# Optimization experiments

Hardware: AMD Instinct MI355X
Metric: run time of the kernel (lower is better)

Reference implementation:

```python
import jax, jax.numpy as jnp
import numpy as np

N = 100000   # nodes
E = 600000   # edges
B = 512      # graphs in batch
H = 128      # hidden dim
ED = 8       # edge feature dim
TWO48 = float(2 ** 48 - 1)


def _w(k, shape, fan_in):
    return jax.random.normal(k, shape, jnp.float32) * (1.0 / np.sqrt(fan_in))


def setup_inputs() -> dict:
    key = jax.random.key(0)
    ks = jax.random.split(key, 32)
    inp = {}
    inp["s_node_ids"] = jax.random.randint(ks[0], (N,), 0, 2 ** 31 - 1, dtype=jnp.int32)
    inp["s_edge_index"] = jax.random.randint(ks[1], (2, E), 0, N, dtype=jnp.int32)
    inp["s_edge_attr"] = jax.random.normal(ks[2], (E, ED), jnp.float32)
    inp["s_batch"] = jnp.sort(jax.random.randint(ks[3], (N,), 0, B, dtype=jnp.int32))
    inp["depth"] = jax.random.uniform(ks[4], (B,), jnp.float32)
    # id_mlp: Linear(1,H) -> ReLU -> Linear(H,H)
    inp["id_w1"] = _w(ks[5], (1, H), 1); inp["id_b1"] = jnp.zeros((H,), jnp.float32)
    inp["id_w2"] = _w(ks[6], (H, H), H); inp["id_b2"] = jnp.zeros((H,), jnp.float32)
    # edge_mlp: Linear(ED,H) -> ReLU -> Linear(H,H)
    inp["ed_w1"] = _w(ks[7], (ED, H), ED); inp["ed_b1"] = jnp.zeros((H,), jnp.float32)
    inp["ed_w2"] = _w(ks[8], (H, H), H); inp["ed_b2"] = jnp.zeros((H,), jnp.float32)
    # GINEConv nn MLPs: Linear(H,H) -> ReLU -> Linear(H,H)
    inp["c1_w1"] = _w(ks[9], (H, H), H); inp["c1_b1"] = jnp.zeros((H,), jnp.float32)
    inp["c1_w2"] = _w(ks[10], (H, H), H); inp["c1_b2"] = jnp.zeros((H,), jnp.float32)
    inp["c2_w1"] = _w(ks[11], (H, H), H); inp["c2_b1"] = jnp.zeros((H,), jnp.float32)
    inp["c2_w2"] = _w(ks[12], (H, H), H); inp["c2_b2"] = jnp.zeros((H,), jnp.float32)
    inp["rg_w1"] = _w(ks[13], (H + 1, H), H + 1); inp["rg_b1"] = jnp.zeros((H,), jnp.float32)
    inp["rg_w2"] = _w(ks[14], (H, 1), H); inp["rg_b2"] = jnp.zeros((1,), jnp.float32)
    return inp


def _mlp2(x, w1, b1, w2, b2):
    return jax.nn.relu(x @ w1 + b1) @ w2 + b2


def _gine(x, src, dst, e, w1, b1, w2, b2):
    # message = ReLU(x_j + e), sum-aggregated at dst; out = nn((1+eps)*x + aggr), eps=0
    msg = jax.nn.relu(x[src] + e)                       # [E, H]
    aggr = jax.ops.segment_sum(msg, dst, num_segments=N)  # [N, H]
    return _mlp2(x + aggr, w1, b1, w2, b2)


def _global_mean(x, batch):
    sums = jax.ops.segment_sum(x, batch, num_segments=B)                          # [B, H]
    cnts = jax.ops.segment_sum(jnp.ones((x.shape[0], 1), x.dtype), batch, num_segments=B)
    return sums / jnp.maximum(cnts, 1.0)


def reference(s_node_ids, s_edge_index, s_edge_attr, s_batch, depth,
              id_w1, id_b1, id_w2, id_b2,
              ed_w1, ed_b1, ed_w2, ed_b2,
              c1_w1, c1_b1, c1_w2, c1_b2,
              c2_w1, c2_b1, c2_w2, c2_b2,
              rg_w1, rg_b1, rg_w2, rg_b2):
    src, dst = s_edge_index[0], s_edge_index[1]
    x0 = jnp.clip(s_node_ids.astype(jnp.float32) / TWO48, 0.0, 1.0)[:, None]  # [N,1]
    x = _mlp2(x0, id_w1, id_b1, id_w2, id_b2)                                 # [N,H]
    e = _mlp2(s_edge_attr, ed_w1, ed_b1, ed_w2, ed_b2)                        # [E,H]
    x = jax.nn.relu(_gine(x, src, dst, e, c1_w1, c1_b1, c1_w2, c1_b2))
    x = jax.nn.relu(_gine(x, src, dst, e, c2_w1, c2_b1, c2_w2, c2_b2))
    rep = jnp.concatenate([_global_mean(x, s_batch), depth[:, None]], axis=1)  # [B,H+1]
    return _mlp2(rep, rg_w1, rg_b1, rg_w2, rg_b2)[:, 0]                        # [B]
```

## Files before the change

kernel.cpp:

```cpp
#include <hip/hip_runtime.h>
#include <hip/hip_bf16.h>

#define N_NODES 100000
#define N_EDGES 600000
#define NB      512
#define H       128
#define ED      8
#define SCAN_CHUNK 1024
#define N_CHUNKS   98

typedef __attribute__((ext_vector_type(8))) short short8;
typedef __attribute__((ext_vector_type(4))) float f32x4;
typedef unsigned short u16;
typedef unsigned int   u32;

static __device__ __forceinline__ u16 f2bf(float f) {
    u32 u = __float_as_uint(f);
    u32 r = u + 0x7fffu + ((u >> 16) & 1u);
    return (u16)(r >> 16);
}
static __device__ __forceinline__ float bf2f(u32 h) {
    return __uint_as_float(h << 16);
}

__global__ __launch_bounds__(256) void pack_all_kernel(
    const float* __restrict__ W0, const float* __restrict__ W1,
    const float* __restrict__ W2, const float* __restrict__ W3,
    const float* __restrict__ W4, const float* __restrict__ W5,
    const float* __restrict__ W6,
    short8* __restrict__ O0, short8* __restrict__ O1,
    short8* __restrict__ O2, short8* __restrict__ O3,
    short8* __restrict__ O4, short8* __restrict__ O5,
    short8* __restrict__ O6)
{
    int gid = blockIdx.x * 256 + threadIdx.x;
    const int total = 512 + 6 * 2048;
    if (gid >= total) return;
    const float* W; short8* O; int Krows, kkmax, slot;
    if (gid < 512) { W = W0; O = O0; Krows = ED; kkmax = 1; slot = gid; }
    else {
        int m = (gid - 512) / 2048;
        slot = (gid - 512) % 2048;
        Krows = H; kkmax = 4;
        switch (m) {
            case 0: W = W1; O = O1; break;
            case 1: W = W2; O = O2; break;
            case 2: W = W3; O = O3; break;
            case 3: W = W4; O = O4; break;
            case 4: W = W5; O = O5; break;
            default: W = W6; O = O6; break;
        }
    }
    int lane = slot & 63;
    int t = slot >> 6;
    int nt = t & 1; t >>= 1;
    int kk = t % kkmax;
    int w  = t / kkmax;
    int quad = lane >> 4, n15 = lane & 15;
    int n = w * 32 + nt * 16 + n15;
    short8 v;
    #pragma unroll
    for (int j = 0; j < 8; j++) {
        int k = kk * 32 + quad * 8 + j;
        v[j] = (k < Krows) ? (short)f2bf(W[k * H + n]) : (short)0;
    }
    O[slot] = v;
}

__global__ __launch_bounds__(256) void hist_kernel(
    const int* __restrict__ edge_index, int* __restrict__ counts)
{
    int e = blockIdx.x * 256 + threadIdx.x;
    if (e < N_EDGES) atomicAdd(&counts[edge_index[N_EDGES + e]], 1);
}

__global__ __launch_bounds__(SCAN_CHUNK) void scan1_kernel(
    const int* __restrict__ counts, int* __restrict__ chunk_scan,
    int* __restrict__ bsum_raw)
{
    __shared__ int s[SCAN_CHUNK];
    int tid = threadIdx.x;
    int gid = blockIdx.x * SCAN_CHUNK + tid;
    int v = counts[gid];
    s[tid] = v;
    __syncthreads();
    #pragma unroll
    for (int off = 1; off < SCAN_CHUNK; off <<= 1) {
        int t = (tid >= off) ? s[tid - off] : 0;
        __syncthreads();
        s[tid] += t;
        __syncthreads();
    }
    chunk_scan[gid] = s[tid] - v;
    if (tid == SCAN_CHUNK - 1) bsum_raw[blockIdx.x] = s[tid];
}

__global__ __launch_bounds__(128) void scan2_kernel(
    const int* __restrict__ bsum_raw, int* __restrict__ bsum_scan)
{
    __shared__ int s[128];
    int tid = threadIdx.x;
    int v = (tid < N_CHUNKS) ? bsum_raw[tid] : 0;
    s[tid] = v;
    __syncthreads();
    #pragma unroll
    for (int off = 1; off < 128; off <<= 1) {
        int t = (tid >= off) ? s[tid - off] : 0;
        __syncthreads();
        s[tid] += t;
        __syncthreads();
    }
    bsum_scan[tid] = s[tid] - v;
}

__global__ __launch_bounds__(256) void fill_kernel(
    const int* __restrict__ edge_index,
    const int* __restrict__ chunk_scan, const int* __restrict__ bsum_scan,
    int* __restrict__ counts, int* __restrict__ src_list,
    int* __restrict__ pos_of)
{
    int e = blockIdx.x * 256 + threadIdx.x;
    if (e >= N_EDGES) return;
    int src = edge_index[e];
    int dst = edge_index[N_EDGES + e];
    int slot = atomicAdd(&counts[dst], -1) - 1;
    int pos = chunk_scan[dst] + bsum_scan[dst >> 10] + slot;
    src_list[pos] = src;
    pos_of[e] = pos;
}

__global__ __launch_bounds__(256) void node_mlp_mfma(
    const int* __restrict__ ids,
    const float* __restrict__ w1, const float* __restrict__ b1,
    const short8* __restrict__ pW2, const float* __restrict__ b2,
    u16* __restrict__ x_out)
{
    __shared__ u16 sH[64 * 136];
    __shared__ float s_x0[64];
    int tid = threadIdx.x;
    int w = tid >> 6, lane = tid & 63, quad = lane >> 4, n15 = lane & 15;
    short8 fW2[4][2];
    #pragma unroll
    for (int kk = 0; kk < 4; kk++) {
        fW2[kk][0] = pW2[((w * 4 + kk) * 2 + 0) * 64 + lane];
        fW2[kk][1] = pW2[((w * 4 + kk) * 2 + 1) * 64 + lane];
    }
    float rb2[2] = { b2[w * 32 + n15], b2[w * 32 + 16 + n15] };
    float w1c = w1[tid & 127], b1c = b1[tid & 127];
    const int ntile = (N_NODES + 63) / 64;
    for (int tile = blockIdx.x; tile < ntile; tile += gridDim.x) {
        int row0 = tile * 64;
        if (tid < 64) {
            int n = row0 + tid;
            float x0 = (n < N_NODES) ? (float)ids[n] / 281474976710655.0f : 0.0f;
            s_x0[tid] = fminf(fmaxf(x0, 0.0f), 1.0f);
        }
        __syncthreads();
        int half = tid >> 7, c = tid & 127;
        #pragma unroll 8
        for (int rr = 0; rr < 32; rr++) {
            int r = half + rr * 2;
            sH[r * 136 + c] = f2bf(fmaxf(s_x0[r] * w1c + b1c, 0.0f));
        }
        __syncthreads();
        f32x4 acc[4][2];
        #pragma unroll
        for (int s = 0; s < 4; s++) { acc[s][0] = (f32x4){0,0,0,0}; acc[s][1] = (f32x4){0,0,0,0}; }
        #pragma unroll
        for (int kk = 0; kk < 4; kk++) {
            #pragma unroll
            for (int s = 0; s < 4; s++) {
                short8 a = *(const short8*)&sH[(s * 16 + n15) * 136 + kk * 32 + quad * 8];
                acc[s][0] = __builtin_amdgcn_mfma_f32_16x16x32_bf16(a, fW2[kk][0], acc[s][0], 0, 0, 0);
                acc[s][1] = __builtin_amdgcn_mfma_f32_16x16x32_bf16(a, fW2[kk][1], acc[s][1], 0, 0, 0);
            }
        }
        #pragma unroll
        for (int s = 0; s < 4; s++)
            #pragma unroll
            for (int nt = 0; nt < 2; nt++) {
                int col = w * 32 + nt * 16 + n15;
                #pragma unroll
                for (int reg = 0; reg < 4; reg++) {
                    int n = row0 + s * 16 + quad * 4 + reg;
                    if (n < N_NODES)
                        x_out[(long)n * H + col] = f2bf(acc[s][nt][reg] + rb2[nt]);
                }
            }
        __syncthreads();
    }
}

__global__ __launch_bounds__(256) void edge_mlp_mfma(
    const float* __restrict__ attr,
    const int* __restrict__ pos_of,
    const short8* __restrict__ pW1, const float* __restrict__ b1,
    const short8* __restrict__ pW2, const float* __restrict__ b2,
    u16* __restrict__ e_perm)
{
    __shared__ u16 sA[64 * 40];
    __shared__ u16 sH[64 * 136];
    __shared__ int sPos[64];
    int tid = threadIdx.x;
    int w = tid >> 6, lane = tid & 63, quad = lane >> 4, n15 = lane & 15;
    short8 fW1[2];
    fW1[0] = pW1[(w * 2 + 0) * 64 + lane];
    fW1[1] = pW1[(w * 2 + 1) * 64 + lane];
    short8 fW2[4][2];
    #pragma unroll
    for (int kk = 0; kk < 4; kk++) {
        fW2[kk][0] = pW2[((w * 4 + kk) * 2 + 0) * 64 + lane];
        fW2[kk][1] = pW2[((w * 4 + kk) * 2 + 1) * 64 + lane];
    }
    float rb1[2] = { b1[w * 32 + n15], b1[w * 32 + 16 + n15] };
    float rb2[2] = { b2[w * 32 + n15], b2[w * 32 + 16 + n15] };
    const int ntile = N_EDGES / 64;
    for (int tile = blockIdx.x; tile < ntile; tile += gridDim.x) {
        int row0 = tile * 64;
        if (tid < 64) sPos[tid] = pos_of[row0 + tid];
        if (tid >= 64 && tid < 192) {
            int t2 = tid - 64;
            int r = t2 >> 1, c4 = (t2 & 1) * 4;
            float4 v = *(const float4*)&attr[(long)(row0 + r) * ED + c4];
            ushort4 o;
            o.x = f2bf(v.x); o.y = f2bf(v.y); o.z = f2bf(v.z); o.w = f2bf(v.w);
            *(ushort4*)&sA[r * 40 + c4] = o;
        } else if (tid >= 192) {
            int idx = tid - 192;
            for (; idx < 192; idx += 64) {
                int r = idx / 3, c8 = 8 + (idx % 3) * 8;
                *(uint4*)&sA[r * 40 + c8] = make_uint4(0, 0, 0, 0);
            }
        }
        __syncthreads();
        f32x4 acc[4][2];
        #pragma unroll
        for (int s = 0; s < 4; s++) { acc[s][0] = (f32x4){0,0,0,0}; acc[s][1] = (f32x4){0,0,0,0}; }
        #pragma unroll
        for (int s = 0; s < 4; s++) {
            short8 a = *(const short8*)&sA[(s * 16 + n15) * 40 + quad * 8];
            acc[s][0] = __builtin_amdgcn_mfma_f32_16x16x32_bf16(a, fW1[0], acc[s][0], 0, 0, 0);
            acc[s][1] = __builtin_amdgcn_mfma_f32_16x16x32_bf16(a, fW1[1], acc[s][1], 0, 0, 0);
        }
        #pragma unroll
        for (int s = 0; s < 4; s++)
            #pragma unroll
            for (int nt = 0; nt < 2; nt++) {
                int col = w * 32 + nt * 16 + n15;
                #pragma unroll
                for (int reg = 0; reg < 4; reg++)
                    sH[(s * 16 + quad * 4 + reg) * 136 + col] =
                        f2bf(fmaxf(acc[s][nt][reg] + rb1[nt], 0.0f));
            }
        __syncthreads();
        #pragma unroll
        for (int s = 0; s < 4; s++) { acc[s][0] = (f32x4){0,0,0,0}; acc[s][1] = (f32x4){0,0,0,0}; }
        #pragma unroll
        for (int kk = 0; kk < 4; kk++) {
            #pragma unroll
            for (int s = 0; s < 4; s++) {
                short8 a = *(const short8*)&sH[(s * 16 + n15) * 136 + kk * 32 + quad * 8];
                acc[s][0] = __builtin_amdgcn_mfma_f32_16x16x32_bf16(a, fW2[kk][0], acc[s][0], 0, 0, 0);
                acc[s][1] = __builtin_amdgcn_mfma_f32_16x16x32_bf16(a, fW2[kk][1], acc[s][1], 0, 0, 0);
            }
        }
        #pragma unroll
        for (int s = 0; s < 4; s++)
            #pragma unroll
            for (int nt = 0; nt < 2; nt++) {
                int col = w * 32 + nt * 16 + n15;
                #pragma unroll
                for (int reg = 0; reg < 4; reg++) {
                    long r = sPos[s * 16 + quad * 4 + reg];
                    e_perm[r * H + col] = f2bf(acc[s][nt][reg] + rb2[nt]);
                }
            }
        __syncthreads();
    }
}

__global__ __launch_bounds__(256) void aggregate_kernel(
    const int* __restrict__ src_list,
    const int* __restrict__ chunk_scan, const int* __restrict__ bsum_scan,
    const u16* __restrict__ e_perm,
    const u16* __restrict__ x,
    u16* __restrict__ xs_out)
{
    int wave = threadIdx.x >> 6;
    int lane = threadIdx.x & 63;
    int fo = lane * 2;
    const int ngroups = N_NODES / 4;
    for (int g = blockIdx.x; g < ngroups; g += gridDim.x) {
        int n = g * 4 + wave;
        int beg = chunk_scan[n]     + bsum_scan[n >> 10];
        int end = chunk_scan[n + 1] + bsum_scan[(n + 1) >> 10];
        float a0 = 0.0f, a1 = 0.0f;
        for (int j0 = beg; j0 < end; j0 += 64) {
            int m = min(64, end - j0);
            int sv = (lane < m) ? src_list[j0 + lane] : 0;
            for (int j = 0; j < m; j++) {
                int src = __shfl(sv, j);
                u32 xv = *(const u32*)&x[(long)src * H + fo];
                u32 ev = *(const u32*)&e_perm[(long)(j0 + j) * H + fo];
                a0 += fmaxf(bf2f(xv & 0xffff) + bf2f(ev & 0xffff), 0.0f);
                a1 += fmaxf(bf2f(xv >> 16)    + bf2f(ev >> 16),    0.0f);
            }
        }
        u32 xself = *(const u32*)&x[(long)n * H + fo];
        float o0 = bf2f(xself & 0xffff) + a0;
        float o1 = bf2f(xself >> 16)    + a1;
        *(u32*)&xs_out[(long)n * H + fo] = (u32)f2bf(o0) | ((u32)f2bf(o1) << 16);
    }
}

__global__ __launch_bounds__(256) void conv_mlp_mfma(
    const u16* __restrict__ xs,
    const short8* __restrict__ pW1, const float* __restrict__ b1,
    const short8* __restrict__ pW2, const float* __restrict__ b2,
    u16* __restrict__ x_out)
{
    __shared__ u16 sA[64 * 136];
    __shared__ u16 sH[64 * 136];
    int tid = threadIdx.x;
    int w = tid >> 6, lane = tid & 63, quad = lane >> 4, n15 = lane & 15;
    short8 fW1[4][2], fW2[4][2];
    #pragma unroll
    for (int kk = 0; kk < 4; kk++) {
        fW1[kk][0] = pW1[((w * 4 + kk) * 2 + 0) * 64 + lane];
        fW1[kk][1] = pW1[((w * 4 + kk) * 2 + 1) * 64 + lane];
        fW2[kk][0] = pW2[((w * 4 + kk) * 2 + 0) * 64 + lane];
        fW2[kk][1] = pW2[((w * 4 + kk) * 2 + 1) * 64 + lane];
    }
    float rb1[2] = { b1[w * 32 + n15], b1[w * 32 + 16 + n15] };
    float rb2[2] = { b2[w * 32 + n15], b2[w * 32 + 16 + n15] };
    const int ntile = (N_NODES + 63) / 64;
    for (int tile = blockIdx.x; tile < ntile; tile += gridDim.x) {
        int row0 = tile * 64;
        for (int idx = tid; idx < 64 * 16; idx += 256) {
            int r = idx >> 4, c8 = (idx & 15) << 3;
            int n = row0 + r;
            uint4 v = make_uint4(0, 0, 0, 0);
            if (n < N_NODES) v = *(const uint4*)&xs[(long)n * H + c8];
            *(uint4*)&sA[r * 136 + c8] = v;
        }
        __syncthreads();
        f32x4 acc[4][2];
        #pragma unroll
        for (int s = 0; s < 4; s++) { acc[s][0] = (f32x4){0,0,0,0}; acc[s][1] = (f32x4){0,0,0,0}; }
        #pragma unroll
        for (int kk = 0; kk < 4; kk++) {
            #pragma unroll
            for (int s = 0; s < 4; s++) {
                short8 a = *(const short8*)&sA[(s * 16 + n15) * 136 + kk * 32 + quad * 8];
                acc[s][0] = __builtin_amdgcn_mfma_f32_16x16x32_bf16(a, fW1[kk][0], acc[s][0], 0, 0, 0);
                acc[s][1] = __builtin_amdgcn_mfma_f32_16x16x32_bf16(a, fW1[kk][1], acc[s][1], 0, 0, 0);
            }
        }
        #pragma unroll
        for (int s = 0; s < 4; s++)
            #pragma unroll
            for (int nt = 0; nt < 2; nt++) {
                int col = w * 32 + nt * 16 + n15;
                #pragma unroll
                for (int reg = 0; reg < 4; reg++)
                    sH[(s * 16 + quad * 4 + reg) * 136 + col] =
                        f2bf(fmaxf(acc[s][nt][reg] + rb1[nt], 0.0f));
            }
        __syncthreads();
        #pragma unroll
        for (int s = 0; s < 4; s++) { acc[s][0] = (f32x4){0,0,0,0}; acc[s][1] = (f32x4){0,0,0,0}; }
        #pragma unroll
        for (int kk = 0; kk < 4; kk++) {
            #pragma unroll
            for (int s = 0; s < 4; s++) {
                short8 a = *(const short8*)&sH[(s * 16 + n15) * 136 + kk * 32 + quad * 8];
                acc[s][0] = __builtin_amdgcn_mfma_f32_16x16x32_bf16(a, fW2[kk][0], acc[s][0], 0, 0, 0);
                acc[s][1] = __builtin_amdgcn_mfma_f32_16x16x32_bf16(a, fW2[kk][1], acc[s][1], 0, 0, 0);
            }
        }
        #pragma unroll
        for (int s = 0; s < 4; s++)
            #pragma unroll
            for (int nt = 0; nt < 2; nt++) {
                int col = w * 32 + nt * 16 + n15;
                #pragma unroll
                for (int reg = 0; reg < 4; reg++) {
                    int n = row0 + s * 16 + quad * 4 + reg;
                    if (n < N_NODES)
                        x_out[(long)n * H + col] = f2bf(fmaxf(acc[s][nt][reg] + rb2[nt], 0.0f));
                }
            }
        __syncthreads();
    }
}

__global__ __launch_bounds__(256) void pool_kernel(
    const u16* __restrict__ x, const int* __restrict__ batch,
    float* __restrict__ sums, float* __restrict__ cnt)
{
    int sg   = threadIdx.x >> 6;
    int lane = threadIdx.x & 63;
    int fo = lane * 2;
    const int nper = (N_NODES + gridDim.x - 1) / gridDim.x;
    int n0 = blockIdx.x * nper;
    int n1 = min(n0 + nper, N_NODES);
    int cur = -1;
    float a0 = 0.0f, a1 = 0.0f, c = 0.0f;
    for (int n = n0 + sg; n < n1; n += 4) {
        int b = batch[n];
        if (b != cur) {
            if (cur >= 0) {
                atomicAdd(&sums[cur * H + fo],     a0);
                atomicAdd(&sums[cur * H + fo + 1], a1);
                if (lane == 0) atomicAdd(&cnt[cur], c);
            }
            a0 = a1 = 0.0f; c = 0.0f; cur = b;
        }
        u32 xv = *(const u32*)&x[(long)n * H + fo];
        a0 += bf2f(xv & 0xffff);
        a1 += bf2f(xv >> 16);
        c += 1.0f;
    }
    if (cur >= 0) {
        atomicAdd(&sums[cur * H + fo],     a0);
        atomicAdd(&sums[cur * H + fo + 1], a1);
        if (lane == 0) atomicAdd(&cnt[cur], c);
    }
}

__global__ __launch_bounds__(128) void regressor_kernel(
    const float* __restrict__ sums, const float* __restrict__ cnt,
    const float* __restrict__ depth,
    const float* __restrict__ w1, const float* __restrict__ b1,
    const float* __restrict__ w2, const float* __restrict__ b2,
    float* __restrict__ out)
{
    __shared__ float s_mean[H];
    __shared__ float s_red[2];
    int b = blockIdx.x;
    int j = threadIdx.x;
    float c = fmaxf(cnt[b], 1.0f);
    s_mean[j] = sums[b * H + j] / c;
    __syncthreads();
    float h = b1[j];
    #pragma unroll 8
    for (int k = 0; k < H; k++) h += s_mean[k] * w1[k * H + j];
    h += depth[b] * w1[H * H + j];
    h = fmaxf(h, 0.0f);
    float p = h * w2[j];
    #pragma unroll
    for (int off = 32; off >= 1; off >>= 1) p += __shfl_down(p, off, 64);
    if ((j & 63) == 0) s_red[j >> 6] = p;
    __syncthreads();
    if (j == 0) out[b] = s_red[0] + s_red[1] + b2[0];
}

extern "C" void kernel_launch(void* const* d_in, const int* in_sizes, int n_in,
                              void* d_out, int out_size, void* d_ws, size_t ws_size,
                              hipStream_t stream)
{
    const int*   ids   = (const int*)  d_in[0];
    const int*   eidx  = (const int*)  d_in[1];
    const float* eattr = (const float*)d_in[2];
    const int*   batch = (const int*)  d_in[3];
    const float* depth = (const float*)d_in[4];
    const float* id_w1 = (const float*)d_in[5];
    const float* id_b1 = (const float*)d_in[6];
    const float* id_w2 = (const float*)d_in[7];
    const float* id_b2 = (const float*)d_in[8];
    const float* ed_w1 = (const float*)d_in[9];
    const float* ed_b1 = (const float*)d_in[10];
    const float* ed_w2 = (const float*)d_in[11];
    const float* ed_b2 = (const float*)d_in[12];
    const float* c1_w1 = (const float*)d_in[13];
    const float* c1_b1 = (const float*)d_in[14];
    const float* c1_w2 = (const float*)d_in[15];
    const float* c1_b2 = (const float*)d_in[16];
    const float* c2_w1 = (const float*)d_in[17];
    const float* c2_b1 = (const float*)d_in[18];
    const float* c2_w2 = (const float*)d_in[19];
    const float* c2_b2 = (const float*)d_in[20];
    const float* rg_w1 = (const float*)d_in[21];
    const float* rg_b1 = (const float*)d_in[22];
    const float* rg_w2 = (const float*)d_in[23];
    const float* rg_b2 = (const float*)d_in[24];

    char* ws = (char*)d_ws;
    u16*   e_buf    = (u16*)  (ws);
    u16*   x_buf    = (u16*)  (ws + 153600000);
    u16*   xs_buf   = (u16*)  (ws + 179200000);
    float* sums_buf = (float*)(ws + 204800000);
    float* cnt_buf  = (float*)(ws + 205062144);
    int*   counts   = (int*)  (ws + 205064192);
    int*   chunk_sc = (int*)  (ws + 205465600);
    int*   bsum_raw = (int*)  (ws + 205867008);
    int*   bsum_sc  = (int*)  (ws + 205867520);
    int*   src_list = (int*)  (ws + 205868032);
    int*   pos_of   = (int*)  (ws + 208268032);
    short8* ed_w1p  = (short8*)(ws + 210668032);
    short8* ed_w2p  = (short8*)(ws + 210676224);
    short8* c1_w1p  = (short8*)(ws + 210708992);
    short8* c1_w2p  = (short8*)(ws + 210741760);
    short8* c2_w1p  = (short8*)(ws + 210774528);
    short8* c2_w2p  = (short8*)(ws + 210807296);
    short8* id_w2p  = (short8*)(ws + 210840064);

    pack_all_kernel<<<50, 256, 0, stream>>>(
        ed_w1, ed_w2, c1_w1, c1_w2, c2_w1, c2_w2, id_w2,
        ed_w1p, ed_w2p, c1_w1p, c1_w2p, c2_w1p, c2_w2p, id_w2p);

    hipMemsetAsync(counts, 0, 401408, stream);
    hist_kernel <<<(N_EDGES + 255) / 256, 256, 0, stream>>>(eidx, counts);
    scan1_kernel<<<N_CHUNKS, SCAN_CHUNK, 0, stream>>>(counts, chunk_sc, bsum_raw);
    scan2_kernel<<<1, 128, 0, stream>>>(bsum_raw, bsum_sc);
    fill_kernel <<<(N_EDGES + 255) / 256, 256, 0, stream>>>(eidx, chunk_sc, bsum_sc,
                                                            counts, src_list, pos_of);

    node_mlp_mfma<<<768, 256, 0, stream>>>(ids, id_w1, id_b1, id_w2p, id_b2, x_buf);
    edge_mlp_mfma<<<2048, 256, 0, stream>>>(eattr, pos_of, ed_w1p, ed_b1, ed_w2p, ed_b2, e_buf);

    aggregate_kernel<<<8192, 256, 0, stream>>>(src_list, chunk_sc, bsum_sc, e_buf, x_buf, xs_buf);
    conv_mlp_mfma<<<1563, 256, 0, stream>>>(xs_buf, c1_w1p, c1_b1, c1_w2p, c1_b2, x_buf);

    aggregate_kernel<<<8192, 256, 0, stream>>>(src_list, chunk_sc, bsum_sc, e_buf, x_buf, xs_buf);
    conv_mlp_mfma<<<1563, 256, 0, stream>>>(xs_buf, c2_w1p, c2_b1, c2_w2p, c2_b2, x_buf);

    hipMemsetAsync(sums_buf, 0, (size_t)(NB * H + NB) * 4, stream);
    pool_kernel<<<2048, 256, 0, stream>>>(x_buf, batch, sums_buf, cnt_buf);
    regressor_kernel<<<NB, 128, 0, stream>>>(sums_buf, cnt_buf, depth,
                                             rg_w1, rg_b1, rg_w2, rg_b2, (float*)d_out);
}
```

Measured before the change: 431.4 us.

## Fuse GINE aggregation into conv MLP kernel and stage output stores through LDS

Merges the separate edge-aggregation kernel and the conv MLP kernel into one gine_fused kernel: each wave gathers and sums messages for 16 nodes straight into the shared-memory A tile, so the intermediate xs buffer is never written to or read back from global memory. It also precomputes CSR row offsets in a small finalize kernel that writes into the counts buffer, and unrolls the gather loop by two with separate accumulators. Node, edge and conv MLP outputs are now staged in LDS and written with 16-byte coalesced stores instead of scattered 2-byte stores. In exchange, the gather now runs inside a 1563-block MFMA kernel with fewer waves in flight than the old 8192-block aggregate, and the reused LDS tile needs extra barriers.

```diff
diff --git a/kernel.cpp b/kernel.cpp
--- a/kernel.cpp
+++ b/kernel.cpp
@@ -129,6 +129,14 @@
     pos_of[e] = pos;
 }
 
+__global__ __launch_bounds__(256) void finalize_offsets(
+    const int* __restrict__ chunk_scan, const int* __restrict__ bsum_scan,
+    int* __restrict__ row_start)
+{
+    int i = blockIdx.x * 256 + threadIdx.x;
+    if (i <= N_NODES) row_start[i] = chunk_scan[i] + bsum_scan[i >> 10];
+}
+
 __global__ __launch_bounds__(256) void node_mlp_mfma(
     const int* __restrict__ ids,
     const float* __restrict__ w1, const float* __restrict__ b1,
@@ -175,18 +183,24 @@
                 acc[s][1] = __builtin_amdgcn_mfma_f32_16x16x32_bf16(a, fW2[kk][1], acc[s][1], 0, 0, 0);
             }
         }
+        __syncthreads();
         #pragma unroll
         for (int s = 0; s < 4; s++)
             #pragma unroll
             for (int nt = 0; nt < 2; nt++) {
                 int col = w * 32 + nt * 16 + n15;
                 #pragma unroll
-                for (int reg = 0; reg < 4; reg++) {
-                    int n = row0 + s * 16 + quad * 4 + reg;
-                    if (n < N_NODES)
-                        x_out[(long)n * H + col] = f2bf(acc[s][nt][reg] + rb2[nt]);
-                }
-            }
+                for (int reg = 0; reg < 4; reg++)
+                    sH[(s * 16 + quad * 4 + reg) * 136 + col] =
+                        f2bf(acc[s][nt][reg] + rb2[nt]);
+            }
+        __syncthreads();
+        for (int idx = tid; idx < 64 * 16; idx += 256) {
+            int r = idx >> 4, c8 = (idx & 15) << 3;
+            int n = row0 + r;
+            if (n < N_NODES)
+                *(uint4*)&x_out[(long)n * H + c8] = *(const uint4*)&sH[r * 136 + c8];
+        }
         __syncthreads();
     }
 }
@@ -264,65 +278,40 @@
                 acc[s][1] = __builtin_amdgcn_mfma_f32_16x16x32_bf16(a, fW2[kk][1], acc[s][1], 0, 0, 0);
             }
         }
+        __syncthreads();
         #pragma unroll
         for (int s = 0; s < 4; s++)
             #pragma unroll
             for (int nt = 0; nt < 2; nt++) {
                 int col = w * 32 + nt * 16 + n15;
                 #pragma unroll
-                for (int reg = 0; reg < 4; reg++) {
-                    long r = sPos[s * 16 + quad * 4 + reg];
-                    e_perm[r * H + col] = f2bf(acc[s][nt][reg] + rb2[nt]);
-                }
-            }
-        __syncthreads();
-    }
-}
-
-__global__ __launch_bounds__(256) void aggregate_kernel(
+                for (int reg = 0; reg < 4; reg++)
+                    sH[(s * 16 + quad * 4 + reg) * 136 + col] =
+                        f2bf(acc[s][nt][reg] + rb2[nt]);
+            }
+        __syncthreads();
+        for (int idx = tid; idx < 64 * 16; idx += 256) {
+            int r = idx >> 4, c8 = (idx & 15) << 3;
+            long rr = sPos[r];
+            *(uint4*)&e_perm[rr * H + c8] = *(const uint4*)&sH[r * 136 + c8];
+        }
+        __syncthreads();
+    }
+}
+
+__global__ __launch_bounds__(256) void gine_fused(
+    const int* __restrict__ row_start,
     const int* __restrict__ src_list,
-    const int* __restrict__ chunk_scan, const int* __restrict__ bsum_scan,
     const u16* __restrict__ e_perm,
     const u16* __restrict__ x,
-    u16* __restrict__ xs_out)
-{
-    int wave = threadIdx.x >> 6;
-    int lane = threadIdx.x & 63;
-    int fo = lane * 2;
-    const int ngroups = N_NODES / 4;
-    for (int g = blockIdx.x; g < ngroups; g += gridDim.x) {
-        int n = g * 4 + wave;
-        int beg = chunk_scan[n]     + bsum_scan[n >> 10];
-        int end = chunk_scan[n + 1] + bsum_scan[(n + 1) >> 10];
-        float a0 = 0.0f, a1 = 0.0f;
-        for (int j0 = beg; j0 < end; j0 += 64) {
-            int m = min(64, end - j0);
-            int sv = (lane < m) ? src_list[j0 + lane] : 0;
-            for (int j = 0; j < m; j++) {
-                int src = __shfl(sv, j);
-                u32 xv = *(const u32*)&x[(long)src * H + fo];
-                u32 ev = *(const u32*)&e_perm[(long)(j0 + j) * H + fo];
-                a0 += fmaxf(bf2f(xv & 0xffff) + bf2f(ev & 0xffff), 0.0f);
-                a1 += fmaxf(bf2f(xv >> 16)    + bf2f(ev >> 16),    0.0f);
-            }
-        }
-        u32 xself = *(const u32*)&x[(long)n * H + fo];
-        float o0 = bf2f(xself & 0xffff) + a0;
-        float o1 = bf2f(xself >> 16)    + a1;
-        *(u32*)&xs_out[(long)n * H + fo] = (u32)f2bf(o0) | ((u32)f2bf(o1) << 16);
-    }
-}
-
-__global__ __launch_bounds__(256) void conv_mlp_mfma(
-    const u16* __restrict__ xs,
     const short8* __restrict__ pW1, const float* __restrict__ b1,
     const short8* __restrict__ pW2, const float* __restrict__ b2,
     u16* __restrict__ x_out)
 {
     __shared__ u16 sA[64 * 136];
-    __shared__ u16 sH[64 * 136];
     int tid = threadIdx.x;
     int w = tid >> 6, lane = tid & 63, quad = lane >> 4, n15 = lane & 15;
+    int fo = lane * 2;
     short8 fW1[4][2], fW2[4][2];
     #pragma unroll
     for (int kk = 0; kk < 4; kk++) {
@@ -333,15 +322,50 @@
     }
     float rb1[2] = { b1[w * 32 + n15], b1[w * 32 + 16 + n15] };
     float rb2[2] = { b2[w * 32 + n15], b2[w * 32 + 16 + n15] };
+    const u16* xb = x + fo;
+    const u16* eb = e_perm + fo;
     const int ntile = (N_NODES + 63) / 64;
     for (int tile = blockIdx.x; tile < ntile; tile += gridDim.x) {
         int row0 = tile * 64;
-        for (int idx = tid; idx < 64 * 16; idx += 256) {
-            int r = idx >> 4, c8 = (idx & 15) << 3;
-            int n = row0 + r;
-            uint4 v = make_uint4(0, 0, 0, 0);
-            if (n < N_NODES) v = *(const uint4*)&xs[(long)n * H + c8];
-            *(uint4*)&sA[r * 136 + c8] = v;
+        int n0 = row0 + w * 16;
+        int rs = row_start[min(n0 + min(lane, 16), N_NODES)];
+        for (int rr = 0; rr < 16; rr++) {
+            int n = n0 + rr;
+            float a0 = 0.0f, a1 = 0.0f, c0 = 0.0f, c1 = 0.0f;
+            if (n < N_NODES) {
+                int beg = __shfl(rs, rr);
+                int end = __shfl(rs, rr + 1);
+                for (int j0 = beg; j0 < end; j0 += 64) {
+                    int m = min(64, end - j0);
+                    int sv = (lane < m) ? src_list[j0 + lane] : 0;
+                    const u16* ej = eb + (long)j0 * H;
+                    int j = 0;
+                    for (; j + 2 <= m; j += 2) {
+                        int s0 = __shfl(sv, j);
+                        int s1 = __shfl(sv, j + 1);
+                        u32 xv0 = *(const u32*)(xb + (long)s0 * H);
+                        u32 ev0 = *(const u32*)(ej + (long)j * H);
+                        u32 xv1 = *(const u32*)(xb + (long)s1 * H);
+                        u32 ev1 = *(const u32*)(ej + (long)(j + 1) * H);
+                        a0 += fmaxf(bf2f(xv0 & 0xffff) + bf2f(ev0 & 0xffff), 0.0f);
+                        a1 += fmaxf(bf2f(xv0 >> 16)    + bf2f(ev0 >> 16),    0.0f);
+                        c0 += fmaxf(bf2f(xv1 & 0xffff) + bf2f(ev1 & 0xffff), 0.0f);
+                        c1 += fmaxf(bf2f(xv1 >> 16)    + bf2f(ev1 >> 16),    0.0f);
+                    }
+                    if (j < m) {
+                        int s0 = __shfl(sv, j);
+                        u32 xv0 = *(const u32*)(xb + (long)s0 * H);
+                        u32 ev0 = *(const u32*)(ej + (long)j * H);
+                        a0 += fmaxf(bf2f(xv0 & 0xffff) + bf2f(ev0 & 0xffff), 0.0f);
+                        a1 += fmaxf(bf2f(xv0 >> 16)    + bf2f(ev0 >> 16),    0.0f);
+                    }
+                }
+                u32 xself = *(const u32*)(xb + (long)n * H);
+                a0 += bf2f(xself & 0xffff) + c0;
+                a1 += bf2f(xself >> 16)    + c1;
+            }
+            u32 o = (u32)f2bf(a0) | ((u32)f2bf(a1) << 16);
+            *(u32*)&sA[(w * 16 + rr) * 136 + fo] = o;
         }
         __syncthreads();
         f32x4 acc[4][2];
@@ -356,6 +380,7 @@
                 acc[s][1] = __builtin_amdgcn_mfma_f32_16x16x32_bf16(a, fW1[kk][1], acc[s][1], 0, 0, 0);
             }
         }
+        __syncthreads();
         #pragma unroll
         for (int s = 0; s < 4; s++)
             #pragma unroll
@@ -363,7 +388,7 @@
                 int col = w * 32 + nt * 16 + n15;
                 #pragma unroll
                 for (int reg = 0; reg < 4; reg++)
-                    sH[(s * 16 + quad * 4 + reg) * 136 + col] =
+                    sA[(s * 16 + quad * 4 + reg) * 136 + col] =
                         f2bf(fmaxf(acc[s][nt][reg] + rb1[nt], 0.0f));
             }
         __syncthreads();
@@ -373,23 +398,29 @@
         for (int kk = 0; kk < 4; kk++) {
             #pragma unroll
             for (int s = 0; s < 4; s++) {
-                short8 a = *(const short8*)&sH[(s * 16 + n15) * 136 + kk * 32 + quad * 8];
+                short8 a = *(const short8*)&sA[(s * 16 + n15) * 136 + kk * 32 + quad * 8];
                 acc[s][0] = __builtin_amdgcn_mfma_f32_16x16x32_bf16(a, fW2[kk][0], acc[s][0], 0, 0, 0);
                 acc[s][1] = __builtin_amdgcn_mfma_f32_16x16x32_bf16(a, fW2[kk][1], acc[s][1], 0, 0, 0);
             }
         }
+        __syncthreads();
         #pragma unroll
         for (int s = 0; s < 4; s++)
             #pragma unroll
             for (int nt = 0; nt < 2; nt++) {
                 int col = w * 32 + nt * 16 + n15;
                 #pragma unroll
-                for (int reg = 0; reg < 4; reg++) {
-                    int n = row0 + s * 16 + quad * 4 + reg;
-                    if (n < N_NODES)
-                        x_out[(long)n * H + col] = f2bf(fmaxf(acc[s][nt][reg] + rb2[nt], 0.0f));
-                }
-            }
+                for (int reg = 0; reg < 4; reg++)
+                    sA[(s * 16 + quad * 4 + reg) * 136 + col] =
+                        f2bf(fmaxf(acc[s][nt][reg] + rb2[nt], 0.0f));
+            }
+        __syncthreads();
+        for (int idx = tid; idx < 64 * 16; idx += 256) {
+            int r = idx >> 4, c8 = (idx & 15) << 3;
+            int n = row0 + r;
+            if (n < N_NODES)
+                *(uint4*)&x_out[(long)n * H + c8] = *(const uint4*)&sA[r * 136 + c8];
+        }
         __syncthreads();
     }
 }
@@ -504,6 +535,7 @@
     short8* c2_w1p  = (short8*)(ws + 210774528);
     short8* c2_w2p  = (short8*)(ws + 210807296);
     short8* id_w2p  = (short8*)(ws + 210840064);
+    int*   row_start = counts;
 
     pack_all_kernel<<<50, 256, 0, stream>>>(
         ed_w1, ed_w2, c1_w1, c1_w2, c2_w1, c2_w2, id_w2,
@@ -515,15 +547,15 @@
     scan2_kernel<<<1, 128, 0, stream>>>(bsum_raw, bsum_sc);
     fill_kernel <<<(N_EDGES + 255) / 256, 256, 0, stream>>>(eidx, chunk_sc, bsum_sc,
                                                             counts, src_list, pos_of);
+    finalize_offsets<<<(N_NODES + 256) / 256, 256, 0, stream>>>(chunk_sc, bsum_sc, row_start);
 
     node_mlp_mfma<<<768, 256, 0, stream>>>(ids, id_w1, id_b1, id_w2p, id_b2, x_buf);
     edge_mlp_mfma<<<2048, 256, 0, stream>>>(eattr, pos_of, ed_w1p, ed_b1, ed_w2p, ed_b2, e_buf);
 
-    aggregate_kernel<<<8192, 256, 0, stream>>>(src_list, chunk_sc, bsum_sc, e_buf, x_buf, xs_buf);
-    conv_mlp_mfma<<<1563, 256, 0, stream>>>(xs_buf, c1_w1p, c1_b1, c1_w2p, c1_b2, x_buf);
-
-    aggregate_kernel<<<8192, 256, 0, stream>>>(src_list, chunk_sc, bsum_sc, e_buf, x_buf, xs_buf);
-    conv_mlp_mfma<<<1563, 256, 0, stream>>>(xs_buf, c2_w1p, c2_b1, c2_w2p, c2_b2, x_buf);
+    gine_fused<<<1563, 256, 0, stream>>>(row_start, src_list, e_buf, x_buf,
+                                         c1_w1p, c1_b1, c1_w2p, c1_b2, xs_buf);
+    gine_fused<<<1563, 256, 0, stream>>>(row_start, src_list, e_buf, xs_buf,
+                                         c2_w1p, c2_b1, c2_w2p, c2_b2, x_buf);
 
     hipMemsetAsync(sums_buf, 0, (size_t)(NB * H + NB) * 4, stream);
     pool_kernel<<<2048, 256, 0, stream>>>(x_buf, batch, sums_buf, cnt_buf);
```

After: 499.4 us. +15.8%, slower.
